# Performance work log

Measured on AMD Instinct MI355X. Metric: run time of the kernel, lower is better.

Reference implementation:

```python
import jax, jax.numpy as jnp
import numpy as np


def setup_inputs() -> dict:
    key = jax.random.key(0)
    k1, k2, k3 = jax.random.split(key, 3)
    B, L, D = 4, 4096, 1024
    inputs = jax.random.normal(k1, (B, L, D), dtype=jnp.float32)
    # nn.Linear(2D, 2D): weight [out=2D, in=2D], bias [2D]
    W_gate = jax.random.normal(k2, (2 * D, 2 * D), dtype=jnp.float32) * (1.0 / np.sqrt(2 * D))
    b_gate = jax.random.normal(k3, (2 * D,), dtype=jnp.float32) * 0.01
    return {"inputs": inputs, "W_gate": W_gate, "b_gate": b_gate}


def reference(inputs, W_gate, b_gate):
    B, L, D = inputs.shape
    # Cumulative average: tril(ones)/arange mask matmul == prefix-mean (linear time)
    denom = jnp.arange(1, L + 1, dtype=inputs.dtype)[None, :, None]  # [1, L, 1]
    average_outputs = jnp.cumsum(inputs, axis=1) / denom  # [B, L, D]
    # Gating linear on concat(inputs, avg): y = x @ W^T + b
    cat = jnp.concatenate([inputs, average_outputs], axis=-1)  # [B, L, 2D]
    gating = jnp.einsum('bld,ed->ble', cat, W_gate) + b_gate  # [B, L, 2D]
    input_gate, forget_gate = jnp.split(gating, 2, axis=-1)
    gating_outputs = (jax.nn.sigmoid(input_gate) * inputs
                      + jax.nn.sigmoid(forget_gate) * average_outputs)
    return gating_outputs, average_outputs
```

## Files before the change

### kernel.cpp

```cpp
#include <hip/hip_runtime.h>

#define B_   4
#define L_   4096
#define D_   1024
#define ROWS (B_ * L_)
#define K2   (2 * D_)
#define BLD  (ROWS * D_)
#define CH   64
#define NC   64

typedef __attribute__((ext_vector_type(8))) short s8v;
typedef __attribute__((ext_vector_type(4))) float f4v;

__device__ __forceinline__ unsigned short f2bf(float f) {
    unsigned int u = __float_as_uint(f);
    u += 0x7FFFu + ((u >> 16) & 1u);
    return (unsigned short)(u >> 16);
}
__device__ __forceinline__ float sigmoidf_(float v) {
    return 1.0f / (1.0f + __expf(-v));
}
__device__ __forceinline__ void llds16(const void* g, void* l) {
    __builtin_amdgcn_global_load_lds(
        (const __attribute__((address_space(1))) unsigned int*)(g),
        (__attribute__((address_space(3))) unsigned int*)(l),
        16, 0, 0);
}


__global__ void prep1(const float4* __restrict__ x4, float4* __restrict__ part4,
                      const float4* __restrict__ W, ushort4* __restrict__ Wbf) {
    int bid = blockIdx.x;
    int t = threadIdx.x;
    if (bid < 256) {
        int c = bid & 63, b = bid >> 6;
        const float4* p = x4 + ((size_t)(b * L_ + c * CH) * 256 + t);
        float4 s; s.x = 0.f; s.y = 0.f; s.z = 0.f; s.w = 0.f;
#pragma unroll 8
        for (int i = 0; i < CH; ++i) {
            float4 v = p[(size_t)i * 256];
            s.x += v.x; s.y += v.y; s.z += v.z; s.w += v.w;
        }
        part4[(size_t)bid * 256 + t] = s;
    } else {
        int i = (bid - 256) * 256 + t;
        float4 v = W[i];
        ushort4 o; o.x = f2bf(v.x); o.y = f2bf(v.y); o.z = f2bf(v.z); o.w = f2bf(v.w);
        Wbf[i] = o;
    }
}

__global__ void apply_scan(const float4* __restrict__ x4, const float4* __restrict__ part4,
                           float4* __restrict__ avg4, ushort4* __restrict__ A4) {
    __shared__ float inv[CH];
    int bid = blockIdx.x;
    int c = bid & 63, b = bid >> 6;
    int t = threadIdx.x;
    if (t < CH) inv[t] = 1.0f / (float)(c * CH + t + 1);

    float4 s; s.x = 0.f; s.y = 0.f; s.z = 0.f; s.w = 0.f;
    for (int cc = 0; cc < c; ++cc) {
        float4 v = part4[((size_t)(b * NC + cc)) * 256 + t];
        s.x += v.x; s.y += v.y; s.z += v.z; s.w += v.w;
    }
    __syncthreads();

    size_t row0 = (size_t)b * L_ + (size_t)c * CH;
    const float4* px = x4 + (row0 * 256 + t);
    float4*       pa = avg4 + (row0 * 256 + t);
    ushort4*      pA = A4 + (row0 * 512 + t);
#pragma unroll 4
    for (int i = 0; i < CH; ++i) {
        float4 v = px[(size_t)i * 256];
        s.x += v.x; s.y += v.y; s.z += v.z; s.w += v.w;
        float r = inv[i];
        float4 av; av.x = s.x * r; av.y = s.y * r; av.z = s.z * r; av.w = s.w * r;
        pa[(size_t)i * 256] = av;
        ushort4 ux; ux.x = f2bf(v.x);  ux.y = f2bf(v.y);  ux.z = f2bf(v.z);  ux.w = f2bf(v.w);
        ushort4 ua; ua.x = f2bf(av.x); ua.y = f2bf(av.y); ua.z = f2bf(av.z); ua.w = f2bf(av.w);
        pA[(size_t)i * 512]       = ux;
        pA[(size_t)i * 512 + 256] = ua;
    }
}

__global__ __launch_bounds__(512, 2) void gemm_gated8(
        const unsigned short* __restrict__ Abf, const unsigned short* __restrict__ Wbf,
        const float* __restrict__ x, const float* __restrict__ avg,
        const float* __restrict__ bg, float* __restrict__ out) {
    __shared__ __attribute__((aligned(16))) unsigned short S[4 * 2 * 8192];

    const int t    = threadIdx.x;
    const int w    = t >> 6;
    const int lane = t & 63;
    const int wm = w >> 1, wn = w & 1;
    const int quad = lane >> 4, lcol = lane & 15;

    const int bid = blockIdx.x;
    const int swz = (bid & 7) * 64 + (bid >> 3);
    const int tileN = swz & 7, tileM = swz >> 3;
    const int row0 = tileM * 256, col0 = tileN * 128;

    f4v acc0[4][4], acc1[4][4];
#pragma unroll
    for (int i = 0; i < 4; ++i)
#pragma unroll
        for (int j = 0; j < 4; ++j)
#pragma unroll
            for (int r = 0; r < 4; ++r) { acc0[i][j][r] = 0.f; acc1[i][j][r] = 0.f; }

    const int qA0 = t, qA1 = 512 + t;
    const int p0 = qA0 ^ ((qA0 >> 3) & 3);
    const int p1 = qA1 ^ ((qA1 >> 3) & 3);
    const int m0 = p0 >> 2, k0e = (p0 & 3) * 8;
    const int m1 = p1 >> 2, k1e = (p1 & 3) * 8;
    const unsigned short* gA0 = Abf + (size_t)(row0 + m0) * K2 + k0e;
    const unsigned short* gA1 = Abf + (size_t)(row0 + m1) * K2 + k1e;
    const unsigned short* gB0 = Wbf + (size_t)(col0 + (m0 & 127) + (m0 >> 7) * 1024) * K2 + k0e;
    const unsigned short* gB1 = Wbf + (size_t)(col0 + (m1 & 127) + (m1 >> 7) * 1024) * K2 + k1e;

    int aoff[4], boff[2][4];
#pragma unroll
    for (int i = 0; i < 4; ++i) {
        int ar = wm * 64 + i * 16 + lcol;
        aoff[i] = ((ar * 64 + quad * 16) ^ (((ar >> 1) & 3) << 4)) >> 1;
    }
#pragma unroll
    for (int h = 0; h < 2; ++h)
#pragma unroll
        for (int j = 0; j < 4; ++j) {
            int br = h * 128 + wn * 64 + j * 16 + lcol;
            boff[h][j] = ((br * 64 + quad * 16) ^ (((br >> 1) & 3) << 4)) >> 1;
        }

#pragma unroll
    for (int tt = 0; tt < 3; ++tt) {
        unsigned short* dA = S + tt * 16384;
        unsigned short* dB = S + tt * 16384 + 8192;
        llds16(gA0 + tt * 32, dA + qA0 * 8);
        llds16(gA1 + tt * 32, dA + qA1 * 8);
        llds16(gB0 + tt * 32, dB + qA0 * 8);
        llds16(gB1 + tt * 32, dB + qA1 * 8);
    }
    asm volatile("s_waitcnt vmcnt(8)" ::: "memory");
    __builtin_amdgcn_s_barrier();

#pragma unroll 4
    for (int tau = 0; tau < 64; ++tau) {
        const unsigned short* bA = S + (tau & 3) * 16384;
        const unsigned short* bB = bA + 8192;
        const int st = tau + 3;
        unsigned short* dA = S + (st & 3) * 16384;
        unsigned short* dB = dA + 8192;
        const bool do_stage = st < 64;
        const int ko = st * 32;

        s8v af[4], bf[4];
#pragma unroll
        for (int i = 0; i < 4; ++i) af[i] = *(const s8v*)(bA + aoff[i]);
#pragma unroll
        for (int j = 0; j < 4; ++j) bf[j] = *(const s8v*)(bB + boff[0][j]);
        if (do_stage) {
            llds16(gA0 + ko, dA + qA0 * 8);
            llds16(gA1 + ko, dA + qA1 * 8);
        }
        __builtin_amdgcn_s_barrier();
        asm volatile("s_waitcnt lgkmcnt(0)");
        __builtin_amdgcn_sched_barrier(0);
        __builtin_amdgcn_s_setprio(1);
#pragma unroll
        for (int i = 0; i < 4; ++i)
#pragma unroll
            for (int j = 0; j < 4; ++j)
                acc0[i][j] = __builtin_amdgcn_mfma_f32_16x16x32_bf16(af[i], bf[j], acc0[i][j], 0, 0, 0);
        __builtin_amdgcn_s_setprio(0);
        __builtin_amdgcn_s_barrier();

        s8v bg2[4];
#pragma unroll
        for (int j = 0; j < 4; ++j) bg2[j] = *(const s8v*)(bB + boff[1][j]);
        if (do_stage) {
            llds16(gB0 + ko, dB + qA0 * 8);
            llds16(gB1 + ko, dB + qA1 * 8);
        }
        if (tau < 61) {
            asm volatile("s_waitcnt vmcnt(8)" ::: "memory");
        } else {
            asm volatile("s_waitcnt vmcnt(0)" ::: "memory");
        }
        __builtin_amdgcn_s_barrier();
        asm volatile("s_waitcnt lgkmcnt(0)");
        __builtin_amdgcn_sched_barrier(0);
        __builtin_amdgcn_s_setprio(1);
#pragma unroll
        for (int i = 0; i < 4; ++i)
#pragma unroll
            for (int j = 0; j < 4; ++j)
                acc1[i][j] = __builtin_amdgcn_mfma_f32_16x16x32_bf16(af[i], bg2[j], acc1[i][j], 0, 0, 0);
        __builtin_amdgcn_s_setprio(0);
        __builtin_amdgcn_s_barrier();
    }

    float b1v[4], b2v[4];
#pragma unroll
    for (int j = 0; j < 4; ++j) {
        int cc = col0 + wn * 64 + j * 16 + lcol;
        b1v[j] = bg[cc];
        b2v[j] = bg[1024 + cc];
    }
#pragma unroll
    for (int i = 0; i < 4; ++i) {
#pragma unroll
        for (int j = 0; j < 4; ++j) {
            int rr = row0 + wm * 64 + i * 16 + quad * 4;
            int cc = col0 + wn * 64 + j * 16 + lcol;
#pragma unroll
            for (int r = 0; r < 4; ++r) {
                size_t off = (size_t)(rr + r) * D_ + cc;
                float gi = sigmoidf_(acc0[i][j][r] + b1v[j]);
                float gf = sigmoidf_(acc1[i][j][r] + b2v[j]);
                out[off] = gi * x[off] + gf * avg[off];
            }
        }
    }
}

extern "C" void kernel_launch(void* const* d_in, const int* in_sizes, int n_in,
                              void* d_out, int out_size, void* d_ws, size_t ws_size,
                              hipStream_t stream) {
    const float* x  = (const float*)d_in[0];
    const float* W  = (const float*)d_in[1];
    const float* bg = (const float*)d_in[2];
    float* out = (float*)d_out;
    float* avg = out + (size_t)BLD;

    char* ws = (char*)d_ws;
    unsigned short* Abf = (unsigned short*)(ws);
    unsigned short* Wbf = (unsigned short*)(ws + (size_t)67108864);
    float4*         prt = (float4*)(ws + (size_t)75497472);

    prep1<<<dim3(4352), dim3(256), 0, stream>>>((const float4*)x, prt,
                                                (const float4*)W, (ushort4*)Wbf);
    apply_scan<<<dim3(256), dim3(256), 0, stream>>>((const float4*)x, prt,
                                                    (float4*)avg, (ushort4*)Abf);
    gemm_gated8<<<dim3(512), dim3(512), 0, stream>>>(Abf, Wbf, x, avg, bg, out);
}
```

Baseline: 373.8 us.

## Halve scan chunk size and merge GEMM half-steps into one barrier phase

The prefix-scan chunk size drops from 64 to 32 rows, which doubles the number of scan blocks to 512 for better GPU occupancy in the prep and apply-scan kernels. The cost is that each apply_scan block now sums up to 127 partials instead of 63. The GEMM main loop now loads both B sub-tiles and issues all four global->LDS copies at once. It then runs both MFMA sets in a single barrier phase, halving the barriers per k-step, and peels the last three iterations into a tail loop without staging. The merged phase needs more live registers for the B fragments and changes how LDS loads overlap with compute.

```diff
diff --git a/kernel.cpp b/kernel.cpp
--- a/kernel.cpp
+++ b/kernel.cpp
@@ -6,8 +6,8 @@
 #define ROWS (B_ * L_)
 #define K2   (2 * D_)
 #define BLD  (ROWS * D_)
-#define CH   64
-#define NC   64
+#define CH   32
+#define NC   128
 
 typedef __attribute__((ext_vector_type(8))) short s8v;
 typedef __attribute__((ext_vector_type(4))) float f4v;
@@ -32,8 +32,8 @@
                       const float4* __restrict__ W, ushort4* __restrict__ Wbf) {
     int bid = blockIdx.x;
     int t = threadIdx.x;
-    if (bid < 256) {
-        int c = bid & 63, b = bid >> 6;
+    if (bid < 512) {
+        int c = bid & 127, b = bid >> 7;
         const float4* p = x4 + ((size_t)(b * L_ + c * CH) * 256 + t);
         float4 s; s.x = 0.f; s.y = 0.f; s.z = 0.f; s.w = 0.f;
 #pragma unroll 8
@@ -43,7 +43,7 @@
         }
         part4[(size_t)bid * 256 + t] = s;
     } else {
-        int i = (bid - 256) * 256 + t;
+        int i = (bid - 512) * 256 + t;
         float4 v = W[i];
         ushort4 o; o.x = f2bf(v.x); o.y = f2bf(v.y); o.z = f2bf(v.z); o.w = f2bf(v.w);
         Wbf[i] = o;
@@ -54,7 +54,7 @@
                            float4* __restrict__ avg4, ushort4* __restrict__ A4) {
     __shared__ float inv[CH];
     int bid = blockIdx.x;
-    int c = bid & 63, b = bid >> 6;
+    int c = bid & 127, b = bid >> 7;
     int t = threadIdx.x;
     if (t < CH) inv[t] = 1.0f / (float)(c * CH + t + 1);
 
@@ -144,25 +144,26 @@
     asm volatile("s_waitcnt vmcnt(8)" ::: "memory");
     __builtin_amdgcn_s_barrier();
 
-#pragma unroll 4
-    for (int tau = 0; tau < 64; ++tau) {
+    for (int tau = 0; tau < 61; ++tau) {
         const unsigned short* bA = S + (tau & 3) * 16384;
         const unsigned short* bB = bA + 8192;
-        const int st = tau + 3;
-        unsigned short* dA = S + (st & 3) * 16384;
+        unsigned short* dA = S + ((tau + 3) & 3) * 16384;
         unsigned short* dB = dA + 8192;
-        const bool do_stage = st < 64;
-        const int ko = st * 32;
-
-        s8v af[4], bf[4];
+        const int ko = (tau + 3) * 32;
+
+        s8v af[4], bf0[4], bf1[4];
 #pragma unroll
         for (int i = 0; i < 4; ++i) af[i] = *(const s8v*)(bA + aoff[i]);
 #pragma unroll
-        for (int j = 0; j < 4; ++j) bf[j] = *(const s8v*)(bB + boff[0][j]);
-        if (do_stage) {
-            llds16(gA0 + ko, dA + qA0 * 8);
-            llds16(gA1 + ko, dA + qA1 * 8);
-        }
+        for (int j = 0; j < 4; ++j) {
+            bf0[j] = *(const s8v*)(bB + boff[0][j]);
+            bf1[j] = *(const s8v*)(bB + boff[1][j]);
+        }
+        llds16(gA0 + ko, dA + qA0 * 8);
+        llds16(gA1 + ko, dA + qA1 * 8);
+        llds16(gB0 + ko, dB + qA0 * 8);
+        llds16(gB1 + ko, dB + qA1 * 8);
+        asm volatile("s_waitcnt vmcnt(8)" ::: "memory");
         __builtin_amdgcn_s_barrier();
         asm volatile("s_waitcnt lgkmcnt(0)");
         __builtin_amdgcn_sched_barrier(0);
@@ -170,23 +171,27 @@
 #pragma unroll
         for (int i = 0; i < 4; ++i)
 #pragma unroll
-            for (int j = 0; j < 4; ++j)
-                acc0[i][j] = __builtin_amdgcn_mfma_f32_16x16x32_bf16(af[i], bf[j], acc0[i][j], 0, 0, 0);
+            for (int j = 0; j < 4; ++j) {
+                acc0[i][j] = __builtin_amdgcn_mfma_f32_16x16x32_bf16(af[i], bf0[j], acc0[i][j], 0, 0, 0);
+                acc1[i][j] = __builtin_amdgcn_mfma_f32_16x16x32_bf16(af[i], bf1[j], acc1[i][j], 0, 0, 0);
+            }
         __builtin_amdgcn_s_setprio(0);
         __builtin_amdgcn_s_barrier();
-
-        s8v bg2[4];
-#pragma unroll
-        for (int j = 0; j < 4; ++j) bg2[j] = *(const s8v*)(bB + boff[1][j]);
-        if (do_stage) {
-            llds16(gB0 + ko, dB + qA0 * 8);
-            llds16(gB1 + ko, dB + qA1 * 8);
-        }
-        if (tau < 61) {
-            asm volatile("s_waitcnt vmcnt(8)" ::: "memory");
-        } else {
-            asm volatile("s_waitcnt vmcnt(0)" ::: "memory");
-        }
+    }
+
+    for (int tau = 61; tau < 64; ++tau) {
+        const unsigned short* bA = S + (tau & 3) * 16384;
+        const unsigned short* bB = bA + 8192;
+
+        s8v af[4], bf0[4], bf1[4];
+#pragma unroll
+        for (int i = 0; i < 4; ++i) af[i] = *(const s8v*)(bA + aoff[i]);
+#pragma unroll
+        for (int j = 0; j < 4; ++j) {
+            bf0[j] = *(const s8v*)(bB + boff[0][j]);
+            bf1[j] = *(const s8v*)(bB + boff[1][j]);
+        }
+        asm volatile("s_waitcnt vmcnt(0)" ::: "memory");
         __builtin_amdgcn_s_barrier();
         asm volatile("s_waitcnt lgkmcnt(0)");
         __builtin_amdgcn_sched_barrier(0);
@@ -194,8 +199,10 @@
 #pragma unroll
         for (int i = 0; i < 4; ++i)
 #pragma unroll
-            for (int j = 0; j < 4; ++j)
-                acc1[i][j] = __builtin_amdgcn_mfma_f32_16x16x32_bf16(af[i], bg2[j], acc1[i][j], 0, 0, 0);
+            for (int j = 0; j < 4; ++j) {
+                acc0[i][j] = __builtin_amdgcn_mfma_f32_16x16x32_bf16(af[i], bf0[j], acc0[i][j], 0, 0, 0);
+                acc1[i][j] = __builtin_amdgcn_mfma_f32_16x16x32_bf16(af[i], bf1[j], acc1[i][j], 0, 0, 0);
+            }
         __builtin_amdgcn_s_setprio(0);
         __builtin_amdgcn_s_barrier();
     }
@@ -238,9 +245,9 @@
     unsigned short* Wbf = (unsigned short*)(ws + (size_t)67108864);
     float4*         prt = (float4*)(ws + (size_t)75497472);
 
-    prep1<<<dim3(4352), dim3(256), 0, stream>>>((const float4*)x, prt,
+    prep1<<<dim3(4608), dim3(256), 0, stream>>>((const float4*)x, prt,
                                                 (const float4*)W, (ushort4*)Wbf);
-    apply_scan<<<dim3(256), dim3(256), 0, stream>>>((const float4*)x, prt,
+    apply_scan<<<dim3(512), dim3(256), 0, stream>>>((const float4*)x, prt,
                                                     (float4*)avg, (ushort4*)Abf);
     gemm_gated8<<<dim3(512), dim3(512), 0, stream>>>(Abf, Wbf, x, avg, bg, out);
 }
```

Measured after the change: 379.2 us. Within noise of the previous version (+1.4%).
